# Kernel optimization log

Measured on AMD Instinct MI355X. Metric: run time of the kernel, lower is better.

Reference implementation:

```python
import jax, jax.numpy as jnp
import numpy as np


def setup_inputs() -> dict:
    key = jax.random.key(0)
    k1, k2 = jax.random.split(key)
    b, s, t, f = 16, 512, 64, 256
    x = jax.random.normal(k1, (b, s, t, f), dtype=jnp.float32)
    w_lambda = jax.random.normal(k2, (f, f), dtype=jnp.float32)
    return {"x": x, "w_lambda": w_lambda}


def reference(x, w_lambda):
    # x: [b, s, t, f]; query = last time step: [b, s, f]
    query = x[:, :, -1, :]
    # Reassociated contraction: (w_lambda @ query) first -> [b, s, f],
    # then dot with x over f -> scores [b, s, t]. Same math as
    # einsum('bstf,fd,bsd->bst') but avoids the O(b*s*t*d) intermediate.
    wq = jnp.einsum('fd,bsd->bsf', w_lambda, query)
    scores = jnp.einsum('bstf,bsf->bst', x, wq)
    weights = jax.nn.softmax(scores, axis=2)
    # Weighted temporal sum -> [b, s, f]
    output = jnp.einsum('bst,bstf->bsf', weights, x)
    return output
```

## Files before the change

### kernel.cpp

```cpp
#include <hip/hip_runtime.h>
#include <hip/hip_bf16.h>
#include <math.h>


#define TT 64
#define FF 256
#define KC 64
#define PAD 68

typedef float v4f __attribute__((ext_vector_type(4)));

__device__ __forceinline__ float4 ntload4(const float* p) {
    v4f t = __builtin_nontemporal_load(reinterpret_cast<const v4f*>(p));
    float4 r; r.x = t.x; r.y = t.y; r.z = t.z; r.w = t.w;
    return r;
}

__global__ __launch_bounds__(256) void wq_gemm(const float* __restrict__ x,
                                               const float* __restrict__ W,
                                               float* __restrict__ wq) {
    __shared__ float qs[KC][PAD];
    __shared__ float ws[KC][PAD];

    const int tid = threadIdx.x;
    const int r0 = (blockIdx.x >> 2) * 64;
    const int f0 = (blockIdx.x & 3) * 64;

    const int tf = tid & 15;
    const int tr = tid >> 4;

    const int sc = tid & 15;
    const int sr = tid >> 4;

    float4 acc[4];
#pragma unroll
    for (int j = 0; j < 4; ++j) acc[j] = make_float4(0.f, 0.f, 0.f, 0.f);

    for (int k0 = 0; k0 < FF; k0 += KC) {
        __syncthreads();
#pragma unroll
        for (int p = 0; p < 4; ++p) {
            int r = sr + 16 * p;
            float4 v = *reinterpret_cast<const float4*>(
                x + (size_t)(r0 + r) * (TT * FF) + (size_t)(TT - 1) * FF + k0 + 4 * sc);
            qs[4 * sc + 0][r] = v.x;
            qs[4 * sc + 1][r] = v.y;
            qs[4 * sc + 2][r] = v.z;
            qs[4 * sc + 3][r] = v.w;
            float4 u = *reinterpret_cast<const float4*>(
                W + (size_t)(f0 + r) * FF + k0 + 4 * sc);
            ws[4 * sc + 0][r] = u.x;
            ws[4 * sc + 1][r] = u.y;
            ws[4 * sc + 2][r] = u.z;
            ws[4 * sc + 3][r] = u.w;
        }
        __syncthreads();

#pragma unroll
        for (int k = 0; k < KC; ++k) {
            float4 qv = *reinterpret_cast<const float4*>(&qs[k][4 * tr]);
            float4 wv = *reinterpret_cast<const float4*>(&ws[k][4 * tf]);
            acc[0].x = fmaf(qv.x, wv.x, acc[0].x);
            acc[0].y = fmaf(qv.x, wv.y, acc[0].y);
            acc[0].z = fmaf(qv.x, wv.z, acc[0].z);
            acc[0].w = fmaf(qv.x, wv.w, acc[0].w);
            acc[1].x = fmaf(qv.y, wv.x, acc[1].x);
            acc[1].y = fmaf(qv.y, wv.y, acc[1].y);
            acc[1].z = fmaf(qv.y, wv.z, acc[1].z);
            acc[1].w = fmaf(qv.y, wv.w, acc[1].w);
            acc[2].x = fmaf(qv.z, wv.x, acc[2].x);
            acc[2].y = fmaf(qv.z, wv.y, acc[2].y);
            acc[2].z = fmaf(qv.z, wv.z, acc[2].z);
            acc[2].w = fmaf(qv.z, wv.w, acc[2].w);
            acc[3].x = fmaf(qv.w, wv.x, acc[3].x);
            acc[3].y = fmaf(qv.w, wv.y, acc[3].y);
            acc[3].z = fmaf(qv.w, wv.z, acc[3].z);
            acc[3].w = fmaf(qv.w, wv.w, acc[3].w);
        }
    }

#pragma unroll
    for (int j = 0; j < 4; ++j)
        *reinterpret_cast<float4*>(
            wq + (size_t)(r0 + 4 * tr + j) * FF + f0 + 4 * tf) = acc[j];
}

__global__ __launch_bounds__(1024, 8) void attn_kernel4(const float* __restrict__ x,
                                                        const float* __restrict__ wq,
                                                        float* __restrict__ out) {
    const int tid  = threadIdx.x;
    const int lane = tid & 63;
    const int w    = tid >> 6;
    const int row  = blockIdx.x;
    const float* xt = x + (size_t)row * (TT * FF);

    __shared__ float sc[TT];
    __shared__ float mbuf[16];
    __shared__ float lbuf[16];
    __shared__ float part[16][FF];

    float4 wqv = *reinterpret_cast<const float4*>(wq + (size_t)row * FF + 4 * lane);

    float4 xv[4];
#pragma unroll
    for (int j = 0; j < 4; ++j)
        xv[j] = ntload4(xt + (size_t)(w * 4 + j) * FF + 4 * lane);

    float p[4];
#pragma unroll
    for (int j = 0; j < 4; ++j)
        p[j] = xv[j].x * wqv.x + xv[j].y * wqv.y + xv[j].z * wqv.z + xv[j].w * wqv.w;

    const bool b5 = (lane & 32) != 0;
    const bool b4 = (lane & 16) != 0;

    float s2[2];
#pragma unroll
    for (int j = 0; j < 2; ++j) {
        float send = b5 ? p[j] : p[j + 2];
        float recv = __shfl_xor(send, 32, 64);
        s2[j] = (b5 ? p[j + 2] : p[j]) + recv;
    }
    float y;
    {
        float send = b4 ? s2[0] : s2[1];
        float recv = __shfl_xor(send, 16, 64);
        y = (b4 ? s2[1] : s2[0]) + recv;
    }
    y += __shfl_xor(y, 8, 64);
    y += __shfl_xor(y, 4, 64);
    y += __shfl_xor(y, 2, 64);
    y += __shfl_xor(y, 1, 64);

    float mw = y;
    mw = fmaxf(mw, __shfl_xor(mw, 16, 64));
    mw = fmaxf(mw, __shfl_xor(mw, 32, 64));

    if ((lane & 15) == 0) sc[w * 4 + (lane >> 4)] = y;
    if (lane == 0) mbuf[w] = mw;
    __syncthreads();

    float m = mbuf[0];
#pragma unroll
    for (int i = 1; i < 16; ++i) m = fmaxf(m, mbuf[i]);

    float wt[4];
    float lw = 0.f;
#pragma unroll
    for (int j = 0; j < 4; ++j) {
        wt[j] = __expf(sc[w * 4 + j] - m);
        lw += wt[j];
    }

    float4 acc = make_float4(0.f, 0.f, 0.f, 0.f);
#pragma unroll
    for (int j = 0; j < 4; ++j) {
        acc.x += wt[j] * xv[j].x;
        acc.y += wt[j] * xv[j].y;
        acc.z += wt[j] * xv[j].z;
        acc.w += wt[j] * xv[j].w;
    }
    *reinterpret_cast<float4*>(&part[w][4 * lane]) = acc;
    if (lane == 0) lbuf[w] = lw;
    __syncthreads();

    if (tid < FF) {
        float l = 0.f;
#pragma unroll
        for (int i = 0; i < 16; ++i) l += lbuf[i];
        float v = 0.f;
#pragma unroll
        for (int i = 0; i < 16; ++i) v += part[i][tid];
        __builtin_nontemporal_store(v / l, out + (size_t)row * FF + tid);
    }
}

__device__ __forceinline__ void attn_row_fb(const float* __restrict__ xt,
                                            float4 wqv,
                                            float* __restrict__ out_row,
                                            int tid) {
    const int lane = tid & 63;
    const int w    = tid >> 6;

    __shared__ float sc[TT];
    __shared__ float part[4][FF];

    float4 xv[16];
#pragma unroll
    for (int j = 0; j < 16; ++j)
        xv[j] = *reinterpret_cast<const float4*>(xt + (size_t)(w * 16 + j) * FF + 4 * lane);

#pragma unroll
    for (int j = 0; j < 16; ++j) {
        float s = xv[j].x * wqv.x + xv[j].y * wqv.y + xv[j].z * wqv.z + xv[j].w * wqv.w;
#pragma unroll
        for (int off = 32; off > 0; off >>= 1)
            s += __shfl_xor(s, off, 64);
        if (lane == 0) sc[w * 16 + j] = s;
    }
    __syncthreads();

    float m = -INFINITY;
#pragma unroll
    for (int t = 0; t < TT; ++t) m = fmaxf(m, sc[t]);
    float l = 0.f;
#pragma unroll
    for (int t = 0; t < TT; ++t) l += __expf(sc[t] - m);

    float4 acc = make_float4(0.f, 0.f, 0.f, 0.f);
#pragma unroll
    for (int j = 0; j < 16; ++j) {
        float wt = __expf(sc[w * 16 + j] - m);
        acc.x += wt * xv[j].x;
        acc.y += wt * xv[j].y;
        acc.z += wt * xv[j].z;
        acc.w += wt * xv[j].w;
    }
    *reinterpret_cast<float4*>(&part[w][4 * lane]) = acc;
    __syncthreads();

    float v = part[0][tid] + part[1][tid] + part[2][tid] + part[3][tid];
    out_row[tid] = v / l;
}

__global__ __launch_bounds__(256) void fused_kernel(const float* __restrict__ x,
                                                    const float* __restrict__ W,
                                                    float* __restrict__ out) {
    const int row = blockIdx.x;
    const int tid = threadIdx.x;
    const int lane = tid & 63;
    const float* xt = x + (size_t)row * (TT * FF);

    __shared__ float q[FF];
    __shared__ float wqs[FF];
    if (tid < 64) {
        float4 v = *reinterpret_cast<const float4*>(xt + (size_t)(TT - 1) * FF + tid * 4);
        *reinterpret_cast<float4*>(&q[tid * 4]) = v;
    }
    __syncthreads();

    float a = 0.f;
    const float* wrow = W + (size_t)tid * FF;
    for (int d0 = 0; d0 < FF; d0 += 4) {
        float4 wv = *reinterpret_cast<const float4*>(wrow + d0);
        float4 qv = *reinterpret_cast<const float4*>(&q[d0]);
        a += wv.x * qv.x + wv.y * qv.y + wv.z * qv.z + wv.w * qv.w;
    }
    wqs[tid] = a;
    __syncthreads();

    float4 wqv = *reinterpret_cast<const float4*>(&wqs[4 * lane]);
    attn_row_fb(xt, wqv, out + (size_t)row * FF, tid);
}

extern "C" void kernel_launch(void* const* d_in, const int* in_sizes, int n_in,
                              void* d_out, int out_size, void* d_ws, size_t ws_size,
                              hipStream_t stream) {
    (void)n_in; (void)out_size;
    const float* x = (const float*)d_in[0];
    const float* W = (const float*)d_in[1];
    float* out = (float*)d_out;

    const int rows = in_sizes[0] / (TT * FF);
    const size_t wq_bytes = (size_t)rows * FF * sizeof(float);

    if (ws_size >= wq_bytes) {
        float* wq = (float*)d_ws;
        wq_gemm<<<(rows / 64) * 4, 256, 0, stream>>>(x, W, wq);
        attn_kernel4<<<rows, 1024, 0, stream>>>(x, wq, out);
    } else {
        fused_kernel<<<rows, 256, 0, stream>>>(x, W, out);
    }
}
```

Measured before the change: 113.4 us.

## Process four rows per attention block with register double-buffered prefetch

Replaces the one-row-per-block attention kernel with a persistent-style kernel where each 1024-thread block handles four consecutive rows. While computing the current row, it prefetches the next row's x tile and wq vector into a second register set, and it alternates shared-memory buffers between rows. The goal is to hide global load latency behind compute and amortize block launch cost. In exchange the grid is four times smaller, which reduces the number of blocks available to hide latency, and shared memory and register use per block roughly double.

```diff
diff --git a/kernel.cpp b/kernel.cpp
--- a/kernel.cpp
+++ b/kernel.cpp
@@ -85,94 +85,91 @@
             wq + (size_t)(r0 + 4 * tr + j) * FF + f0 + 4 * tf) = acc[j];
 }
 
-__global__ __launch_bounds__(1024, 8) void attn_kernel4(const float* __restrict__ x,
-                                                        const float* __restrict__ wq,
-                                                        float* __restrict__ out) {
-    const int tid  = threadIdx.x;
-    const int lane = tid & 63;
-    const int w    = tid >> 6;
-    const int row  = blockIdx.x;
-    const float* xt = x + (size_t)row * (TT * FF);
-
-    __shared__ float sc[TT];
-    __shared__ float mbuf[16];
-    __shared__ float lbuf[16];
-    __shared__ float part[16][FF];
-
-    float4 wqv = *reinterpret_cast<const float4*>(wq + (size_t)row * FF + 4 * lane);
-
-    float4 xv[4];
-#pragma unroll
-    for (int j = 0; j < 4; ++j)
-        xv[j] = ntload4(xt + (size_t)(w * 4 + j) * FF + 4 * lane);
-
-    float p[4];
-#pragma unroll
-    for (int j = 0; j < 4; ++j)
-        p[j] = xv[j].x * wqv.x + xv[j].y * wqv.y + xv[j].z * wqv.z + xv[j].w * wqv.w;
-
+__device__ __forceinline__ void fold4(const float p[4], int lane, float& y, float& mw) {
     const bool b5 = (lane & 32) != 0;
     const bool b4 = (lane & 16) != 0;
-
-    float s2[2];
-#pragma unroll
-    for (int j = 0; j < 2; ++j) {
-        float send = b5 ? p[j] : p[j + 2];
-        float recv = __shfl_xor(send, 32, 64);
-        s2[j] = (b5 ? p[j + 2] : p[j]) + recv;
-    }
-    float y;
-    {
-        float send = b4 ? s2[0] : s2[1];
-        float recv = __shfl_xor(send, 16, 64);
-        y = (b4 ? s2[1] : s2[0]) + recv;
-    }
+    float s2a, s2b;
+    { float send = b5 ? p[0] : p[2]; float recv = __shfl_xor(send, 32, 64); s2a = (b5 ? p[2] : p[0]) + recv; }
+    { float send = b5 ? p[1] : p[3]; float recv = __shfl_xor(send, 32, 64); s2b = (b5 ? p[3] : p[1]) + recv; }
+    { float send = b4 ? s2a : s2b; float recv = __shfl_xor(send, 16, 64); y = (b4 ? s2b : s2a) + recv; }
     y += __shfl_xor(y, 8, 64);
     y += __shfl_xor(y, 4, 64);
     y += __shfl_xor(y, 2, 64);
     y += __shfl_xor(y, 1, 64);
-
-    float mw = y;
+    mw = y;
     mw = fmaxf(mw, __shfl_xor(mw, 16, 64));
     mw = fmaxf(mw, __shfl_xor(mw, 32, 64));
-
-    if ((lane & 15) == 0) sc[w * 4 + (lane >> 4)] = y;
-    if (lane == 0) mbuf[w] = mw;
-    __syncthreads();
-
-    float m = mbuf[0];
-#pragma unroll
-    for (int i = 1; i < 16; ++i) m = fmaxf(m, mbuf[i]);
-
-    float wt[4];
-    float lw = 0.f;
-#pragma unroll
-    for (int j = 0; j < 4; ++j) {
-        wt[j] = __expf(sc[w * 4 + j] - m);
-        lw += wt[j];
-    }
-
-    float4 acc = make_float4(0.f, 0.f, 0.f, 0.f);
-#pragma unroll
-    for (int j = 0; j < 4; ++j) {
-        acc.x += wt[j] * xv[j].x;
-        acc.y += wt[j] * xv[j].y;
-        acc.z += wt[j] * xv[j].z;
-        acc.w += wt[j] * xv[j].w;
-    }
-    *reinterpret_cast<float4*>(&part[w][4 * lane]) = acc;
-    if (lane == 0) lbuf[w] = lw;
-    __syncthreads();
-
-    if (tid < FF) {
-        float l = 0.f;
-#pragma unroll
-        for (int i = 0; i < 16; ++i) l += lbuf[i];
-        float v = 0.f;
-#pragma unroll
-        for (int i = 0; i < 16; ++i) v += part[i][tid];
-        __builtin_nontemporal_store(v / l, out + (size_t)row * FF + tid);
-    }
+}
+
+__global__ __launch_bounds__(1024, 8) void attn_pipe(const float* __restrict__ x,
+                                                     const float* __restrict__ wq,
+                                                     float* __restrict__ out) {
+    const int tid  = threadIdx.x;
+    const int lane = tid & 63;
+    const int w    = tid >> 6;
+    const size_t r0 = (size_t)blockIdx.x * 4;
+
+    __shared__ float sc[2][TT];
+    __shared__ float mb[2][16];
+    __shared__ float lb[2][16];
+    __shared__ float part[2][16][FF];
+
+    float4 xvA[4], xvB[4];
+    float4 wqA, wqB;
+
+    const float* xt0 = x + r0 * (TT * FF) + (size_t)(w * 4) * FF + 4 * lane;
+
+#pragma unroll
+    for (int j = 0; j < 4; ++j) xvA[j] = ntload4(xt0 + (size_t)j * FF);
+    wqA = *reinterpret_cast<const float4*>(wq + r0 * FF + 4 * lane);
+
+#define ROW(r, XV, WQ, NXV, NWQ, PF) do {                                        \
+    if (PF) {                                                                    \
+        const float* xtn = xt0 + (size_t)((r) + 1) * (TT * FF);                  \
+        _Pragma("unroll")                                                        \
+        for (int j = 0; j < 4; ++j) NXV[j] = ntload4(xtn + (size_t)j * FF);      \
+        NWQ = *reinterpret_cast<const float4*>(wq + (r0 + (r) + 1) * FF + 4 * lane); \
+    }                                                                            \
+    float p[4];                                                                  \
+    _Pragma("unroll")                                                            \
+    for (int j = 0; j < 4; ++j)                                                  \
+        p[j] = XV[j].x * WQ.x + XV[j].y * WQ.y + XV[j].z * WQ.z + XV[j].w * WQ.w;\
+    float y, mw;                                                                 \
+    fold4(p, lane, y, mw);                                                       \
+    if ((lane & 15) == 0) sc[(r) & 1][w * 4 + (lane >> 4)] = y;                  \
+    if (lane == 0) mb[(r) & 1][w] = mw;                                          \
+    __syncthreads();                                                             \
+    float m = mb[(r) & 1][0];                                                    \
+    _Pragma("unroll")                                                            \
+    for (int i = 1; i < 16; ++i) m = fmaxf(m, mb[(r) & 1][i]);                   \
+    float wt[4]; float lw = 0.f;                                                 \
+    _Pragma("unroll")                                                            \
+    for (int j = 0; j < 4; ++j) { wt[j] = __expf(sc[(r) & 1][w * 4 + j] - m); lw += wt[j]; } \
+    float4 acc = make_float4(0.f, 0.f, 0.f, 0.f);                                \
+    _Pragma("unroll")                                                            \
+    for (int j = 0; j < 4; ++j) {                                                \
+        acc.x += wt[j] * XV[j].x; acc.y += wt[j] * XV[j].y;                      \
+        acc.z += wt[j] * XV[j].z; acc.w += wt[j] * XV[j].w;                      \
+    }                                                                            \
+    *reinterpret_cast<float4*>(&part[(r) & 1][w][4 * lane]) = acc;               \
+    if (lane == 0) lb[(r) & 1][w] = lw;                                          \
+    __syncthreads();                                                             \
+    if (tid < FF) {                                                              \
+        float l = 0.f;                                                           \
+        _Pragma("unroll")                                                        \
+        for (int i = 0; i < 16; ++i) l += lb[(r) & 1][i];                        \
+        float v = 0.f;                                                           \
+        _Pragma("unroll")                                                        \
+        for (int i = 0; i < 16; ++i) v += part[(r) & 1][i][tid];                 \
+        __builtin_nontemporal_store(v / l, out + (r0 + (r)) * FF + tid);         \
+    }                                                                            \
+} while (0)
+
+    ROW(0, xvA, wqA, xvB, wqB, true);
+    ROW(1, xvB, wqB, xvA, wqA, true);
+    ROW(2, xvA, wqA, xvB, wqB, true);
+    ROW(3, xvB, wqB, xvA, wqA, false);
+#undef ROW
 }
 
 __device__ __forceinline__ void attn_row_fb(const float* __restrict__ xt,
@@ -182,8 +179,8 @@
     const int lane = tid & 63;
     const int w    = tid >> 6;
 
-    __shared__ float sc[TT];
-    __shared__ float part[4][FF];
+    __shared__ float scf[TT];
+    __shared__ float partf[4][FF];
 
     float4 xv[16];
 #pragma unroll
@@ -196,30 +193,30 @@
 #pragma unroll
         for (int off = 32; off > 0; off >>= 1)
             s += __shfl_xor(s, off, 64);
-        if (lane == 0) sc[w * 16 + j] = s;
+        if (lane == 0) scf[w * 16 + j] = s;
     }
     __syncthreads();
 
     float m = -INFINITY;
 #pragma unroll
-    for (int t = 0; t < TT; ++t) m = fmaxf(m, sc[t]);
+    for (int t = 0; t < TT; ++t) m = fmaxf(m, scf[t]);
     float l = 0.f;
 #pragma unroll
-    for (int t = 0; t < TT; ++t) l += __expf(sc[t] - m);
+    for (int t = 0; t < TT; ++t) l += __expf(scf[t] - m);
 
     float4 acc = make_float4(0.f, 0.f, 0.f, 0.f);
 #pragma unroll
     for (int j = 0; j < 16; ++j) {
-        float wt = __expf(sc[w * 16 + j] - m);
+        float wt = __expf(scf[w * 16 + j] - m);
         acc.x += wt * xv[j].x;
         acc.y += wt * xv[j].y;
         acc.z += wt * xv[j].z;
         acc.w += wt * xv[j].w;
     }
-    *reinterpret_cast<float4*>(&part[w][4 * lane]) = acc;
-    __syncthreads();
-
-    float v = part[0][tid] + part[1][tid] + part[2][tid] + part[3][tid];
+    *reinterpret_cast<float4*>(&partf[w][4 * lane]) = acc;
+    __syncthreads();
+
+    float v = partf[0][tid] + partf[1][tid] + partf[2][tid] + partf[3][tid];
     out_row[tid] = v / l;
 }
 
@@ -267,7 +264,7 @@
     if (ws_size >= wq_bytes) {
         float* wq = (float*)d_ws;
         wq_gemm<<<(rows / 64) * 4, 256, 0, stream>>>(x, W, wq);
-        attn_kernel4<<<rows, 1024, 0, stream>>>(x, wq, out);
+        attn_pipe<<<rows / 4, 1024, 0, stream>>>(x, wq, out);
     } else {
         fused_kernel<<<rows, 256, 0, stream>>>(x, W, out);
     }
```

Measured after the change: 134.6 us. 1.19x slower.
